# Performance work log

Measured on AMD Instinct MI355X. Metric: run time of the kernel, lower is better.

## Reference

```python
import jax, jax.numpy as jnp
import numpy as np

B, N, FEAT, HID, CTX = 16384, 7, 512, 256, 256
COMB = N * HID + CTX  # 2048


def setup_inputs() -> dict:
    key = jax.random.key(0)
    ks = jax.random.split(key, 20)
    s = lambda k, shape, sc=0.05: jax.random.normal(k, shape, dtype=jnp.float32) * sc
    adj = jax.random.randint(ks[1], (N, N), 0, 2).astype(jnp.float32)
    # guarantee self-loops so no row is fully masked (still exercise nan_to_num path robustly)
    adj = jnp.maximum(adj, jnp.eye(N, dtype=jnp.float32))
    return {
        "node_feats": jax.random.normal(ks[0], (B, N, FEAT), dtype=jnp.float32),
        "adj": adj,
        "context": jax.random.normal(ks[2], (B, CTX), dtype=jnp.float32),
        "base_preds": jax.random.normal(ks[3], (B, 5), dtype=jnp.float32),
        "W1": s(ks[4], (HID, FEAT)),
        "a1": s(ks[5], (1, 2 * HID)),
        "W2": s(ks[6], (HID, HID)),
        "a2": s(ks[7], (1, 2 * HID)),
        "wh1_w": s(ks[8], (32, COMB)), "wh1_b": s(ks[9], (32,)),
        "wh2_w": s(ks[10], (16, 32)), "wh2_b": s(ks[11], (16,)),
        "wh3_w": s(ks[12], (5, 16)), "wh3_b": s(ks[13], (5,)),
        "rh1_w": s(ks[14], (16, COMB)), "rh1_b": s(ks[15], (16,)),
        "rh2_w": s(ks[16], (1, 16)), "rh2_b": s(ks[17], (1,)),
    }


def _gat_layer(x, adj, W, a):
    # x: (B, N, in_dim); W: (D, in_dim); a: (1, 2D)
    h = jnp.einsum('bni,di->bnd', x, W)  # (B, N, D)
    D = W.shape[0]
    # a([h_i, h_j]) == h_i @ a[:, :D] + h_j @ a[:, D:]
    s_i = h @ a[0, :D]   # (B, N)
    s_j = h @ a[0, D:]   # (B, N)
    e = s_i[:, :, None] + s_j[:, None, :]          # (B, N, N)
    e = jax.nn.leaky_relu(e, negative_slope=0.2)
    e = jnp.where(adj[None] == 0, -jnp.inf, e)
    alpha = jax.nn.softmax(e, axis=-1)
    alpha = jnp.nan_to_num(alpha, nan=0.0)
    out = jnp.einsum('bij,bjd->bid', alpha, h)     # (B, N, D)
    return out, alpha


def reference(node_feats, adj, context, base_preds, W1, a1, W2, a2,
              wh1_w, wh1_b, wh2_w, wh2_b, wh3_w, wh3_b,
              rh1_w, rh1_b, rh2_w, rh2_b):
    h, _attn1 = _gat_layer(node_feats, adj, W1, a1)
    h = jax.nn.relu(h)
    h, attn2 = _gat_layer(h, adj, W2, a2)
    h = jax.nn.relu(h)
    graph_embed = h.reshape(h.shape[0], -1)                 # (B, N*D)
    combined = jnp.concatenate([graph_embed, context], -1)  # (B, COMB)
    # weight head (dropout is inference-mode identity)
    t = jax.nn.relu(combined @ wh1_w.T + wh1_b)
    t = jax.nn.relu(t @ wh2_w.T + wh2_b)
    raw_weights = t @ wh3_w.T + wh3_b                       # (B, 5)
    weights = jax.nn.softmax(raw_weights, axis=-1)
    weighted_pred = jnp.sum(weights * base_preds, axis=-1)  # (B,)
    r = jnp.tanh(combined @ rh1_w.T + rh1_b)
    residual = (r @ rh2_w.T + rh2_b)[:, 0] * 0.05
    pred = jnp.maximum(weighted_pred + residual, 0.05)
    return pred, weights, attn2
```

## Files before the change

### kernel.cpp

```cpp
#include <hip/hip_runtime.h>

#define B_SZ 16384
#define NN 7
#define HID 256
#define COMB 2048

typedef __attribute__((ext_vector_type(8))) short short8;
typedef __attribute__((ext_vector_type(4))) float floatx4;
typedef __attribute__((ext_vector_type(4))) unsigned short ushortx4;
typedef unsigned short us;

__device__ __forceinline__ float bf2f(us u) {
    union { unsigned int i; float f; } v; v.i = ((unsigned int)u) << 16; return v.f;
}
__device__ __forceinline__ us f2bf(float f) {
    union { unsigned int i; float f; } v; v.f = f;
    return (us)((v.i + 0x7FFFu + ((v.i >> 16) & 1u)) >> 16);
}
__device__ __forceinline__ us f2bf_fast(float f) {
    union { unsigned int i; float f; } v; v.f = f;
    return (us)((v.i + 0x8000u) >> 16);
}
__device__ __forceinline__ void gl_lds16(const us* g, us* l) {
    __builtin_amdgcn_global_load_lds(
        (const __attribute__((address_space(1))) unsigned int*)g,
        (__attribute__((address_space(3))) unsigned int*)l, 16, 0, 0);
}

__global__ __launch_bounds__(256) void pack_weights(const float* __restrict__ W1,
                                                    const float* __restrict__ W2,
                                                    const float* __restrict__ wh1,
                                                    const float* __restrict__ rh1,
                                                    us* __restrict__ dst) {
    int i = (blockIdx.x * 256 + threadIdx.x) * 4;
    if (i >= 294912) return;
    const float* src; int off;
    if (i < 131072)      { src = W1;  off = i; }
    else if (i < 196608) { src = W2;  off = i - 131072; }
    else if (i < 262144) { src = wh1; off = i - 196608; }
    else                 { src = rh1; off = i - 262144; }
    floatx4 v = *(const floatx4*)(src + off);
    ushortx4 o = {f2bf(v[0]), f2bf(v[1]), f2bf(v[2]), f2bf(v[3])};
    *(ushortx4*)(dst + i) = o;
}

template <int SRC_STRIDE, bool WRITE_ALPHA>
__device__ __forceinline__ void attn_graph(const us* hb, const float* adjs, const float* avec,
                                           us* dst, int dstStride, float* alpha_dst, int lane) {
    float hv[NN][4];
#pragma unroll
    for (int n = 0; n < NN; ++n) {
        ushortx4 r = *(const ushortx4*)(hb + n * SRC_STRIDE + lane * 4);
        hv[n][0] = bf2f(r[0]); hv[n][1] = bf2f(r[1]);
        hv[n][2] = bf2f(r[2]); hv[n][3] = bf2f(r[3]);
    }
    floatx4 ai = *(const floatx4*)(avec + lane * 4);
    floatx4 aj = *(const floatx4*)(avec + HID + lane * 4);
    float si[NN], sj[NN];
#pragma unroll
    for (int n = 0; n < NN; ++n) {
        float pi = hv[n][0] * ai[0] + hv[n][1] * ai[1] + hv[n][2] * ai[2] + hv[n][3] * ai[3];
        float pj = hv[n][0] * aj[0] + hv[n][1] * aj[1] + hv[n][2] * aj[2] + hv[n][3] * aj[3];
#pragma unroll
        for (int off = 32; off; off >>= 1) {
            pi += __shfl_xor(pi, off);
            pj += __shfl_xor(pj, off);
        }
        si[n] = pi; sj[n] = pj;
    }
    const int j = lane & 7;
    float sjm = sj[0];
    if (j == 1) sjm = sj[1];
    if (j == 2) sjm = sj[2];
    if (j == 3) sjm = sj[3];
    if (j == 4) sjm = sj[4];
    if (j == 5) sjm = sj[5];
    if (j == 6) sjm = sj[6];
    const int jc = (j < 7) ? j : 0;
    float alpha[NN];
#pragma unroll
    for (int i = 0; i < NN; ++i) {
        float x = si[i] + sjm;
        x = (x >= 0.f) ? x : 0.2f * x;
        bool ok = (j < 7) && (adjs[i * 7 + jc] != 0.f);
        float e = ok ? x : -1e30f;
        float m = e;
        m = fmaxf(m, __shfl_xor(m, 1, 8));
        m = fmaxf(m, __shfl_xor(m, 2, 8));
        m = fmaxf(m, __shfl_xor(m, 4, 8));
        float ex = ok ? __expf(e - m) : 0.f;
        float s = ex;
        s += __shfl_xor(s, 1, 8);
        s += __shfl_xor(s, 2, 8);
        s += __shfl_xor(s, 4, 8);
        alpha[i] = (s > 0.f) ? ex * __frcp_rn(s) : 0.f;
    }
    if (WRITE_ALPHA && lane < 7) {
#pragma unroll
        for (int i = 0; i < NN; ++i) alpha_dst[i * NN + lane] = alpha[i];
    }
#pragma unroll
    for (int i = 0; i < NN; ++i) {
        floatx4 o = (floatx4){0.f, 0.f, 0.f, 0.f};
#pragma unroll
        for (int jj = 0; jj < NN; ++jj) {
            float a = __shfl(alpha[i], jj, 8);
            o[0] += a * hv[jj][0]; o[1] += a * hv[jj][1];
            o[2] += a * hv[jj][2]; o[3] += a * hv[jj][3];
        }
        ushortx4 st = {f2bf(fmaxf(o[0], 0.f)), f2bf(fmaxf(o[1], 0.f)),
                       f2bf(fmaxf(o[2], 0.f)), f2bf(fmaxf(o[3], 0.f))};
        *(ushortx4*)(dst + i * dstStride + lane * 4) = st;
    }
}


__global__ __launch_bounds__(512, 4) void fused_g1(const float* __restrict__ Af,
                                                   const us* __restrict__ W1b,
                                                   const float* __restrict__ adj,
                                                   const float* __restrict__ avec,
                                                   us* __restrict__ x2g) {
    __shared__ __attribute__((aligned(16))) us As[4096];
    __shared__ __attribute__((aligned(16))) us hs[56 * 264];
    __shared__ float adjs[52];
    const int tid = threadIdx.x;
    const int wave = tid >> 6, lane = tid & 63;
    const int quad = lane >> 4, m16 = lane & 15;
    const long rowBase = (long)blockIdx.x * 56;
    if (tid < 49) adjs[tid] = adj[tid];

    floatx4 acc[4][2];
#pragma unroll
    for (int rt = 0; rt < 4; ++rt)
#pragma unroll
        for (int ct = 0; ct < 2; ++ct) acc[rt][ct] = (floatx4){0.f, 0.f, 0.f, 0.f};

    const int r = tid >> 3, kq8 = tid & 7;
    long rowA = rowBase + r; if (rowA > 114687) rowA = 114687;
    const float* aptr = Af + rowA * 512 + kq8 * 8;
    us* wdst = &As[((r >> 3) * 64 + (r & 7) * 8 + kq8) * 8];
    const int colb = wave * 32;

    for (int s = 0; s < 8; ++s) {
        const int k0 = s * 64;
        floatx4 v0 = *(const floatx4*)(aptr + k0);
        floatx4 v1 = *(const floatx4*)(aptr + k0 + 4);
        short8 sv;
        sv[0] = f2bf_fast(v0[0]); sv[1] = f2bf_fast(v0[1]);
        sv[2] = f2bf_fast(v0[2]); sv[3] = f2bf_fast(v0[3]);
        sv[4] = f2bf_fast(v1[0]); sv[5] = f2bf_fast(v1[1]);
        sv[6] = f2bf_fast(v1[2]); sv[7] = f2bf_fast(v1[3]);
        *(short8*)wdst = sv;
        __syncthreads();
#pragma unroll
        for (int t = 0; t < 2; ++t) {
            short8 b0 = *(const short8*)(W1b + (long)(colb + m16) * 512 + k0 + t * 32 + quad * 8);
            short8 b1 = *(const short8*)(W1b + (long)(colb + 16 + m16) * 512 + k0 + t * 32 + quad * 8);
            short8 a[4];
#pragma unroll
            for (int rt = 0; rt < 4; ++rt)
                a[rt] = *(const short8*)&As[((rt * 2 + (m16 >> 3)) * 64 + (m16 & 7) * 8 + t * 4 + quad) * 8];
#pragma unroll
            for (int rt = 0; rt < 4; ++rt) {
                acc[rt][0] = __builtin_amdgcn_mfma_f32_16x16x32_bf16(a[rt], b0, acc[rt][0], 0, 0, 0);
                acc[rt][1] = __builtin_amdgcn_mfma_f32_16x16x32_bf16(a[rt], b1, acc[rt][1], 0, 0, 0);
            }
        }
        __syncthreads();
    }
#pragma unroll
    for (int rt = 0; rt < 4; ++rt)
#pragma unroll
        for (int ct = 0; ct < 2; ++ct)
#pragma unroll
            for (int i = 0; i < 4; ++i) {
                int row = rt * 16 + quad * 4 + i;
                if (row < 56) hs[row * 264 + wave * 32 + ct * 16 + m16] = f2bf(acc[rt][ct][i]);
            }
    __syncthreads();
    attn_graph<264, false>(&hs[wave * 7 * 264], adjs, avec,
                           x2g + ((long)blockIdx.x * 64 + wave * 7) * 256, 256, nullptr, lane);
}

__global__ __launch_bounds__(512, 4) void fused_rest(const us* __restrict__ x2g,
                                                     const us* __restrict__ W2b,
                                                     const us* __restrict__ Whb,
                                                     const float* __restrict__ adj,
                                                     const float* __restrict__ avec,
                                                     const float* __restrict__ context,
                                                     const float* __restrict__ wh1_b,
                                                     const float* __restrict__ wh2_w,
                                                     const float* __restrict__ wh2_b,
                                                     const float* __restrict__ wh3_w,
                                                     const float* __restrict__ wh3_b,
                                                     const float* __restrict__ rh1_b,
                                                     const float* __restrict__ rh2_w,
                                                     const float* __restrict__ rh2_b,
                                                     const float* __restrict__ base_preds,
                                                     float* __restrict__ out) {
    __shared__ __attribute__((aligned(16))) us As[4096];
    __shared__ __attribute__((aligned(16))) us hs[56 * 264];
    __shared__ __attribute__((aligned(16))) us ctxs[8 * 264];
    __shared__ float red[8 * 384];
    __shared__ float fin[384];
    __shared__ float adjs[52];
    const int tid = threadIdx.x;
    const int wave = tid >> 6, lane = tid & 63;
    const int quad = lane >> 4, m16 = lane & 15;
    const long rowBaseX = (long)blockIdx.x * 64;
    const long gbase = (long)blockIdx.x * 8;
    if (tid < 49) adjs[tid] = adj[tid];
    {
        int cr = tid >> 6, c4 = (tid & 63) * 4;
        floatx4 cv = *(const floatx4*)(context + (gbase + cr) * 256 + c4);
        ushortx4 st = {f2bf(cv[0]), f2bf(cv[1]), f2bf(cv[2]), f2bf(cv[3])};
        *(ushortx4*)&ctxs[cr * 264 + c4] = st;
    }

    floatx4 acc[4][2];
#pragma unroll
    for (int rt = 0; rt < 4; ++rt)
#pragma unroll
        for (int ct = 0; ct < 2; ++ct) acc[rt][ct] = (floatx4){0.f, 0.f, 0.f, 0.f};
    const int colb = wave * 32;

    for (int s = 0; s < 4; ++s) {
        const int k0 = s * 64;
        gl_lds16(x2g + (rowBaseX + wave * 8 + (lane >> 3)) * 256 + k0 + (lane & 7) * 8,
                 &As[wave * 512]);
        __syncthreads();
#pragma unroll
        for (int t = 0; t < 2; ++t) {
            short8 b0 = *(const short8*)(W2b + (long)(colb + m16) * 256 + k0 + t * 32 + quad * 8);
            short8 b1 = *(const short8*)(W2b + (long)(colb + 16 + m16) * 256 + k0 + t * 32 + quad * 8);
            short8 a[4];
#pragma unroll
            for (int rt = 0; rt < 4; ++rt)
                a[rt] = *(const short8*)&As[((rt * 2 + (m16 >> 3)) * 64 + (m16 & 7) * 8 + t * 4 + quad) * 8];
#pragma unroll
            for (int rt = 0; rt < 4; ++rt) {
                acc[rt][0] = __builtin_amdgcn_mfma_f32_16x16x32_bf16(a[rt], b0, acc[rt][0], 0, 0, 0);
                acc[rt][1] = __builtin_amdgcn_mfma_f32_16x16x32_bf16(a[rt], b1, acc[rt][1], 0, 0, 0);
            }
        }
        __syncthreads();
    }
#pragma unroll
    for (int rt = 0; rt < 4; ++rt)
#pragma unroll
        for (int ct = 0; ct < 2; ++ct)
#pragma unroll
            for (int i = 0; i < 4; ++i) {
                int row = rt * 16 + quad * 4 + i;
                if (row < 56) hs[row * 264 + wave * 32 + ct * 16 + m16] = f2bf(acc[rt][ct][i]);
            }
    __syncthreads();
    float* alf = out + 6 * B_SZ;
    attn_graph<264, true>(&hs[wave * 7 * 264], adjs, avec,
                          &hs[wave * 7 * 264], 264, alf + (gbase + wave) * 49, lane);
    __syncthreads();
    floatx4 acc3[3];
#pragma unroll
    for (int ct = 0; ct < 3; ++ct) acc3[ct] = (floatx4){0.f, 0.f, 0.f, 0.f};
    const int g = m16 & 7;
#pragma unroll
    for (int s2 = 0; s2 < 8; ++s2) {
        const int kk = s2 * 32;
        short8 a;
        if (wave < 7) a = *(const short8*)&hs[(g * 7 + wave) * 264 + kk + quad * 8];
        else          a = *(const short8*)&ctxs[g * 264 + kk + quad * 8];
#pragma unroll
        for (int ct = 0; ct < 3; ++ct) {
            short8 bh = *(const short8*)(Whb + (long)(ct * 16 + m16) * COMB + wave * 256 + kk + quad * 8);
            acc3[ct] = __builtin_amdgcn_mfma_f32_16x16x32_bf16(a, bh, acc3[ct], 0, 0, 0);
        }
    }
#pragma unroll
    for (int ct = 0; ct < 3; ++ct)
#pragma unroll
        for (int i = 0; i < 4; ++i) {
            int g2 = quad * 4 + i;
            if (g2 < 8) red[wave * 384 + g2 * 48 + ct * 16 + m16] = acc3[ct][i];
        }
    __syncthreads();
    if (tid < 384) {
        float ssum = 0.f;
#pragma unroll
        for (int w = 0; w < 8; ++w) ssum += red[w * 384 + tid];
        fin[tid] = ssum;
    }
    __syncthreads();
    if (tid < 8) {
        const long b = gbase + tid;
        const float* g48 = &fin[tid * 48];
        float t1[32], r1[16];
#pragma unroll
        for (int k = 0; k < 32; ++k) t1[k] = fmaxf(g48[k] + wh1_b[k], 0.f);
#pragma unroll
        for (int k = 0; k < 16; ++k) r1[k] = tanhf(g48[32 + k] + rh1_b[k]);
        float t2[16];
#pragma unroll
        for (int jj = 0; jj < 16; ++jj) {
            float s = wh2_b[jj];
            for (int k = 0; k < 32; ++k) s += wh2_w[jj * 32 + k] * t1[k];
            t2[jj] = fmaxf(s, 0.f);
        }
        float rw[5], m = -1e30f;
#pragma unroll
        for (int o = 0; o < 5; ++o) {
            float s = wh3_b[o];
            for (int jj = 0; jj < 16; ++jj) s += wh3_w[o * 16 + jj] * t2[jj];
            rw[o] = s; m = fmaxf(m, s);
        }
        float se = 0.f;
#pragma unroll
        for (int o = 0; o < 5; ++o) { rw[o] = __expf(rw[o] - m); se += rw[o]; }
        float inv = 1.f / se, wp = 0.f;
#pragma unroll
        for (int o = 0; o < 5; ++o) {
            float w = rw[o] * inv;
            out[B_SZ + b * 5 + o] = w;
            wp += w * base_preds[b * 5 + o];
        }
        float rs = rh2_b[0];
#pragma unroll
        for (int k = 0; k < 16; ++k) rs += rh2_w[k] * r1[k];
        out[b] = fmaxf(wp + rs * 0.05f, 0.05f);
    }
}

extern "C" void kernel_launch(void* const* d_in, const int* in_sizes, int n_in,
                              void* d_out, int out_size, void* d_ws, size_t ws_size,
                              hipStream_t stream) {
    const float* node_feats = (const float*)d_in[0];
    const float* adj        = (const float*)d_in[1];
    const float* context    = (const float*)d_in[2];
    const float* base_preds = (const float*)d_in[3];
    const float* W1         = (const float*)d_in[4];
    const float* a1         = (const float*)d_in[5];
    const float* W2         = (const float*)d_in[6];
    const float* a2         = (const float*)d_in[7];
    const float* wh1_w = (const float*)d_in[8];
    const float* wh1_b = (const float*)d_in[9];
    const float* wh2_w = (const float*)d_in[10];
    const float* wh2_b = (const float*)d_in[11];
    const float* wh3_w = (const float*)d_in[12];
    const float* wh3_b = (const float*)d_in[13];
    const float* rh1_w = (const float*)d_in[14];
    const float* rh1_b = (const float*)d_in[15];
    const float* rh2_w = (const float*)d_in[16];
    const float* rh2_b = (const float*)d_in[17];
    float* out = (float*)d_out;

    char* ws = (char*)d_ws;
    const size_t X2B = (size_t)2048 * 64 * 256 * 2;
    us* x2  = (us*)ws;
    us* W1b = (us*)(ws + X2B);
    us* W2b = W1b + 131072;
    us* Whb = W2b + 65536;

    pack_weights<<<288, 256, 0, stream>>>(W1, W2, wh1_w, rh1_w, W1b);

    fused_g1<<<2048, 512, 0, stream>>>(node_feats, W1b, adj, a1, x2);

    fused_rest<<<2048, 512, 0, stream>>>(x2, W2b, Whb, adj, a2, context,
                                         wh1_b, wh2_w, wh2_b, wh3_w, wh3_b,
                                         rh1_b, rh2_w, rh2_b, base_preds, out);
}
```

Baseline: 536.7 us.

## Fuse both GAT layers and heads into one kernel with swizzled in-LDS intermediates

Merges the two-kernel pipeline into a single kernel that keeps the layer-1 GAT output in shared memory instead of round-tripping it through a global bf16 buffer. Layer-2 and the head GEMM then read directly from LDS. The shared layout uses XOR swizzling, and the layer-1 A loads are double-buffered and prefetched so one barrier per K step is dropped. Context is converted on the fly, and the tiny MLP tail is parallelised across 64 lanes instead of 8 threads. Risks include higher register and LDS pressure under the new occupancy target, and the long serial chain inside one block.

```diff
diff --git a/kernel.cpp b/kernel.cpp
--- a/kernel.cpp
+++ b/kernel.cpp
@@ -21,10 +21,12 @@
     union { unsigned int i; float f; } v; v.f = f;
     return (us)((v.i + 0x8000u) >> 16);
 }
-__device__ __forceinline__ void gl_lds16(const us* g, us* l) {
-    __builtin_amdgcn_global_load_lds(
-        (const __attribute__((address_space(1))) unsigned int*)g,
-        (__attribute__((address_space(3))) unsigned int*)l, 16, 0, 0);
+
+__device__ __forceinline__ int hoff(int r, int k8) {
+    return ((r >> 3) << 8) | ((r & 7) << 5) | (k8 & 24) | ((k8 ^ r) & 7);
+}
+__device__ __forceinline__ int aoff(int r, int k8) {
+    return ((r >> 3) << 6) | ((r & 7) << 3) | ((k8 ^ r) & 7);
 }
 
 __global__ __launch_bounds__(256) void pack_weights(const float* __restrict__ W1,
@@ -44,15 +46,16 @@
     *(ushortx4*)(dst + i) = o;
 }
 
-template <int SRC_STRIDE, bool WRITE_ALPHA>
-__device__ __forceinline__ void attn_graph(const us* hb, const float* adjs, const float* avec,
-                                           us* dst, int dstStride, float* alpha_dst, int lane) {
+template <bool WRITE_ALPHA>
+__device__ __forceinline__ void attn_graph(us* hs, int r0, const float* adjs, const float* avec,
+                                           float* alpha_dst, int lane) {
+    const int k8 = lane >> 1, sub = (lane & 1) * 4;
     float hv[NN][4];
 #pragma unroll
     for (int n = 0; n < NN; ++n) {
-        ushortx4 r = *(const ushortx4*)(hb + n * SRC_STRIDE + lane * 4);
-        hv[n][0] = bf2f(r[0]); hv[n][1] = bf2f(r[1]);
-        hv[n][2] = bf2f(r[2]); hv[n][3] = bf2f(r[3]);
+        ushortx4 rr = *(const ushortx4*)(hs + hoff(r0 + n, k8) * 8 + sub);
+        hv[n][0] = bf2f(rr[0]); hv[n][1] = bf2f(rr[1]);
+        hv[n][2] = bf2f(rr[2]); hv[n][3] = bf2f(rr[3]);
     }
     floatx4 ai = *(const floatx4*)(avec + lane * 4);
     floatx4 aj = *(const floatx4*)(avec + HID + lane * 4);
@@ -110,24 +113,45 @@
         }
         ushortx4 st = {f2bf(fmaxf(o[0], 0.f)), f2bf(fmaxf(o[1], 0.f)),
                        f2bf(fmaxf(o[2], 0.f)), f2bf(fmaxf(o[3], 0.f))};
-        *(ushortx4*)(dst + i * dstStride + lane * 4) = st;
-    }
-}
-
-
-__global__ __launch_bounds__(512, 4) void fused_g1(const float* __restrict__ Af,
-                                                   const us* __restrict__ W1b,
-                                                   const float* __restrict__ adj,
-                                                   const float* __restrict__ avec,
-                                                   us* __restrict__ x2g) {
-    __shared__ __attribute__((aligned(16))) us As[4096];
-    __shared__ __attribute__((aligned(16))) us hs[56 * 264];
+        *(ushortx4*)(hs + hoff(r0 + i, k8) * 8 + sub) = st;
+    }
+}
+
+__device__ __forceinline__ void cwrite(us* hs, floatx4 (&acc)[4][2], int wave, int quad, int m16) {
+#pragma unroll
+    for (int rt = 0; rt < 4; ++rt)
+#pragma unroll
+        for (int ct = 0; ct < 2; ++ct)
+#pragma unroll
+            for (int i = 0; i < 4; ++i) {
+                int row = rt * 16 + quad * 4 + i;
+                if (row < 56)
+                    hs[hoff(row, wave * 4 + ct * 2 + (m16 >> 3)) * 8 + (m16 & 7)] =
+                        f2bf(acc[rt][ct][i]);
+            }
+}
+
+__global__ __launch_bounds__(512, 6) void fused_all(
+    const float* __restrict__ Af, const us* __restrict__ W1b, const us* __restrict__ W2b,
+    const us* __restrict__ Whb, const float* __restrict__ adj, const float* __restrict__ a1v,
+    const float* __restrict__ a2v, const float* __restrict__ context,
+    const float* __restrict__ wh1_b, const float* __restrict__ wh2_w,
+    const float* __restrict__ wh2_b, const float* __restrict__ wh3_w,
+    const float* __restrict__ wh3_b, const float* __restrict__ rh1_b,
+    const float* __restrict__ rh2_w, const float* __restrict__ rh2_b,
+    const float* __restrict__ base_preds, float* __restrict__ out) {
+    __shared__ __attribute__((aligned(16))) us hs[16384];
+    __shared__ __attribute__((aligned(16))) char ubuf[16384];
     __shared__ float adjs[52];
+    us* As = (us*)ubuf;
+    float* red = (float*)ubuf;
+    float* fin = red + 3072;
     const int tid = threadIdx.x;
     const int wave = tid >> 6, lane = tid & 63;
     const int quad = lane >> 4, m16 = lane & 15;
-    const long rowBase = (long)blockIdx.x * 56;
+    const long gbase = (long)blockIdx.x * 8;
     if (tid < 49) adjs[tid] = adj[tid];
+    *(ushortx4*)(hs + 14336 + tid * 4) = (ushortx4){0, 0, 0, 0};
 
     floatx4 acc[4][2];
 #pragma unroll
@@ -136,22 +160,28 @@
         for (int ct = 0; ct < 2; ++ct) acc[rt][ct] = (floatx4){0.f, 0.f, 0.f, 0.f};
 
     const int r = tid >> 3, kq8 = tid & 7;
-    long rowA = rowBase + r; if (rowA > 114687) rowA = 114687;
+    long rowA = gbase * 7 + r; if (rowA > 114687) rowA = 114687;
     const float* aptr = Af + rowA * 512 + kq8 * 8;
-    us* wdst = &As[((r >> 3) * 64 + (r & 7) * 8 + kq8) * 8];
+    us* wdst = As + aoff(r, kq8) * 8;
     const int colb = wave * 32;
 
+    floatx4 v0 = *(const floatx4*)aptr;
+    floatx4 v1 = *(const floatx4*)(aptr + 4);
+#pragma unroll
     for (int s = 0; s < 8; ++s) {
-        const int k0 = s * 64;
-        floatx4 v0 = *(const floatx4*)(aptr + k0);
-        floatx4 v1 = *(const floatx4*)(aptr + k0 + 4);
         short8 sv;
         sv[0] = f2bf_fast(v0[0]); sv[1] = f2bf_fast(v0[1]);
         sv[2] = f2bf_fast(v0[2]); sv[3] = f2bf_fast(v0[3]);
         sv[4] = f2bf_fast(v1[0]); sv[5] = f2bf_fast(v1[1]);
         sv[6] = f2bf_fast(v1[2]); sv[7] = f2bf_fast(v1[3]);
-        *(short8*)wdst = sv;
+        if (s < 7) {
+            v0 = *(const floatx4*)(aptr + (s + 1) * 64);
+            v1 = *(const floatx4*)(aptr + (s + 1) * 64 + 4);
+        }
+        *(short8*)(wdst + (s & 1) * 4096) = sv;
         __syncthreads();
+        const us* Ab = As + (s & 1) * 4096;
+        const int k0 = s * 64;
 #pragma unroll
         for (int t = 0; t < 2; ++t) {
             short8 b0 = *(const short8*)(W1b + (long)(colb + m16) * 512 + k0 + t * 32 + quad * 8);
@@ -159,76 +189,26 @@
             short8 a[4];
 #pragma unroll
             for (int rt = 0; rt < 4; ++rt)
-                a[rt] = *(const short8*)&As[((rt * 2 + (m16 >> 3)) * 64 + (m16 & 7) * 8 + t * 4 + quad) * 8];
+                a[rt] = *(const short8*)(Ab + aoff(rt * 16 + m16, t * 4 + quad) * 8);
 #pragma unroll
             for (int rt = 0; rt < 4; ++rt) {
                 acc[rt][0] = __builtin_amdgcn_mfma_f32_16x16x32_bf16(a[rt], b0, acc[rt][0], 0, 0, 0);
                 acc[rt][1] = __builtin_amdgcn_mfma_f32_16x16x32_bf16(a[rt], b1, acc[rt][1], 0, 0, 0);
             }
         }
-        __syncthreads();
-    }
+    }
+    cwrite(hs, acc, wave, quad, m16);
+    __syncthreads();
+    attn_graph<false>(hs, wave * NN, adjs, a1v, nullptr, lane);
+    __syncthreads();
+
 #pragma unroll
     for (int rt = 0; rt < 4; ++rt)
 #pragma unroll
-        for (int ct = 0; ct < 2; ++ct)
-#pragma unroll
-            for (int i = 0; i < 4; ++i) {
-                int row = rt * 16 + quad * 4 + i;
-                if (row < 56) hs[row * 264 + wave * 32 + ct * 16 + m16] = f2bf(acc[rt][ct][i]);
-            }
-    __syncthreads();
-    attn_graph<264, false>(&hs[wave * 7 * 264], adjs, avec,
-                           x2g + ((long)blockIdx.x * 64 + wave * 7) * 256, 256, nullptr, lane);
-}
-
-__global__ __launch_bounds__(512, 4) void fused_rest(const us* __restrict__ x2g,
-                                                     const us* __restrict__ W2b,
-                                                     const us* __restrict__ Whb,
-                                                     const float* __restrict__ adj,
-                                                     const float* __restrict__ avec,
-                                                     const float* __restrict__ context,
-                                                     const float* __restrict__ wh1_b,
-                                                     const float* __restrict__ wh2_w,
-                                                     const float* __restrict__ wh2_b,
-                                                     const float* __restrict__ wh3_w,
-                                                     const float* __restrict__ wh3_b,
-                                                     const float* __restrict__ rh1_b,
-                                                     const float* __restrict__ rh2_w,
-                                                     const float* __restrict__ rh2_b,
-                                                     const float* __restrict__ base_preds,
-                                                     float* __restrict__ out) {
-    __shared__ __attribute__((aligned(16))) us As[4096];
-    __shared__ __attribute__((aligned(16))) us hs[56 * 264];
-    __shared__ __attribute__((aligned(16))) us ctxs[8 * 264];
-    __shared__ float red[8 * 384];
-    __shared__ float fin[384];
-    __shared__ float adjs[52];
-    const int tid = threadIdx.x;
-    const int wave = tid >> 6, lane = tid & 63;
-    const int quad = lane >> 4, m16 = lane & 15;
-    const long rowBaseX = (long)blockIdx.x * 64;
-    const long gbase = (long)blockIdx.x * 8;
-    if (tid < 49) adjs[tid] = adj[tid];
-    {
-        int cr = tid >> 6, c4 = (tid & 63) * 4;
-        floatx4 cv = *(const floatx4*)(context + (gbase + cr) * 256 + c4);
-        ushortx4 st = {f2bf(cv[0]), f2bf(cv[1]), f2bf(cv[2]), f2bf(cv[3])};
-        *(ushortx4*)&ctxs[cr * 264 + c4] = st;
-    }
-
-    floatx4 acc[4][2];
-#pragma unroll
-    for (int rt = 0; rt < 4; ++rt)
-#pragma unroll
         for (int ct = 0; ct < 2; ++ct) acc[rt][ct] = (floatx4){0.f, 0.f, 0.f, 0.f};
-    const int colb = wave * 32;
-
+#pragma unroll
     for (int s = 0; s < 4; ++s) {
         const int k0 = s * 64;
-        gl_lds16(x2g + (rowBaseX + wave * 8 + (lane >> 3)) * 256 + k0 + (lane & 7) * 8,
-                 &As[wave * 512]);
-        __syncthreads();
 #pragma unroll
         for (int t = 0; t < 2; ++t) {
             short8 b0 = *(const short8*)(W2b + (long)(colb + m16) * 256 + k0 + t * 32 + quad * 8);
@@ -236,29 +216,20 @@
             short8 a[4];
 #pragma unroll
             for (int rt = 0; rt < 4; ++rt)
-                a[rt] = *(const short8*)&As[((rt * 2 + (m16 >> 3)) * 64 + (m16 & 7) * 8 + t * 4 + quad) * 8];
+                a[rt] = *(const short8*)(hs + hoff(rt * 16 + m16, s * 8 + t * 4 + quad) * 8);
 #pragma unroll
             for (int rt = 0; rt < 4; ++rt) {
                 acc[rt][0] = __builtin_amdgcn_mfma_f32_16x16x32_bf16(a[rt], b0, acc[rt][0], 0, 0, 0);
                 acc[rt][1] = __builtin_amdgcn_mfma_f32_16x16x32_bf16(a[rt], b1, acc[rt][1], 0, 0, 0);
             }
         }
-        __syncthreads();
-    }
-#pragma unroll
-    for (int rt = 0; rt < 4; ++rt)
-#pragma unroll
-        for (int ct = 0; ct < 2; ++ct)
-#pragma unroll
-            for (int i = 0; i < 4; ++i) {
-                int row = rt * 16 + quad * 4 + i;
-                if (row < 56) hs[row * 264 + wave * 32 + ct * 16 + m16] = f2bf(acc[rt][ct][i]);
-            }
-    __syncthreads();
-    float* alf = out + 6 * B_SZ;
-    attn_graph<264, true>(&hs[wave * 7 * 264], adjs, avec,
-                          &hs[wave * 7 * 264], 264, alf + (gbase + wave) * 49, lane);
-    __syncthreads();
+    }
+    __syncthreads();
+    cwrite(hs, acc, wave, quad, m16);
+    __syncthreads();
+    attn_graph<true>(hs, wave * NN, adjs, a2v, out + 6 * B_SZ + (gbase + wave) * 49, lane);
+    __syncthreads();
+
     floatx4 acc3[3];
 #pragma unroll
     for (int ct = 0; ct < 3; ++ct) acc3[ct] = (floatx4){0.f, 0.f, 0.f, 0.f};
@@ -267,8 +238,17 @@
     for (int s2 = 0; s2 < 8; ++s2) {
         const int kk = s2 * 32;
         short8 a;
-        if (wave < 7) a = *(const short8*)&hs[(g * 7 + wave) * 264 + kk + quad * 8];
-        else          a = *(const short8*)&ctxs[g * 264 + kk + quad * 8];
+        if (wave < 7) {
+            a = *(const short8*)(hs + hoff(g * NN + wave, s2 * 4 + quad) * 8);
+        } else {
+            const float* cp = context + (gbase + g) * 256 + kk + quad * 8;
+            floatx4 c0 = *(const floatx4*)cp;
+            floatx4 c1 = *(const floatx4*)(cp + 4);
+            a[0] = (short)f2bf(c0[0]); a[1] = (short)f2bf(c0[1]);
+            a[2] = (short)f2bf(c0[2]); a[3] = (short)f2bf(c0[3]);
+            a[4] = (short)f2bf(c1[0]); a[5] = (short)f2bf(c1[1]);
+            a[6] = (short)f2bf(c1[2]); a[7] = (short)f2bf(c1[3]);
+        }
 #pragma unroll
         for (int ct = 0; ct < 3; ++ct) {
             short8 bh = *(const short8*)(Whb + (long)(ct * 16 + m16) * COMB + wave * 256 + kk + quad * 8);
@@ -290,42 +270,71 @@
         fin[tid] = ssum;
     }
     __syncthreads();
-    if (tid < 8) {
-        const long b = gbase + tid;
-        const float* g48 = &fin[tid * 48];
-        float t1[32], r1[16];
-#pragma unroll
-        for (int k = 0; k < 32; ++k) t1[k] = fmaxf(g48[k] + wh1_b[k], 0.f);
-#pragma unroll
-        for (int k = 0; k < 16; ++k) r1[k] = tanhf(g48[32 + k] + rh1_b[k]);
-        float t2[16];
-#pragma unroll
-        for (int jj = 0; jj < 16; ++jj) {
-            float s = wh2_b[jj];
-            for (int k = 0; k < 32; ++k) s += wh2_w[jj * 32 + k] * t1[k];
-            t2[jj] = fmaxf(s, 0.f);
-        }
-        float rw[5], m = -1e30f;
-#pragma unroll
-        for (int o = 0; o < 5; ++o) {
-            float s = wh3_b[o];
-            for (int jj = 0; jj < 16; ++jj) s += wh3_w[o * 16 + jj] * t2[jj];
-            rw[o] = s; m = fmaxf(m, s);
-        }
-        float se = 0.f;
-#pragma unroll
-        for (int o = 0; o < 5; ++o) { rw[o] = __expf(rw[o] - m); se += rw[o]; }
-        float inv = 1.f / se, wp = 0.f;
-#pragma unroll
-        for (int o = 0; o < 5; ++o) {
-            float w = rw[o] * inv;
-            out[B_SZ + b * 5 + o] = w;
-            wp += w * base_preds[b * 5 + o];
-        }
-        float rs = rh2_b[0];
-#pragma unroll
-        for (int k = 0; k < 16; ++k) rs += rh2_w[k] * r1[k];
-        out[b] = fmaxf(wp + rs * 0.05f, 0.05f);
+
+    const int fj = lane & 7, fg = lane >> 3;
+    const long fb = gbase + fg;
+    float rp = 0.f;
+    float* t1s = red;
+    float* t2s = red + 256;
+    if (tid < 64) {
+        const float* g48 = fin + fg * 48;
+#pragma unroll
+        for (int x = 0; x < 4; ++x) {
+            int k = fj * 4 + x;
+            t1s[fg * 32 + k] = fmaxf(g48[k] + wh1_b[k], 0.f);
+        }
+#pragma unroll
+        for (int x = 0; x < 2; ++x) {
+            int k = fj * 2 + x;
+            float rv = tanhf(g48[32 + k] + rh1_b[k]);
+            rp += rh2_w[k] * rv;
+        }
+    }
+    __syncthreads();
+    if (tid < 64) {
+        float s0 = wh2_b[fj * 2], s1 = wh2_b[fj * 2 + 1];
+#pragma unroll
+        for (int k = 0; k < 32; ++k) {
+            float tv = t1s[fg * 32 + k];
+            s0 += wh2_w[(fj * 2) * 32 + k] * tv;
+            s1 += wh2_w[(fj * 2 + 1) * 32 + k] * tv;
+        }
+        t2s[fg * 16 + fj * 2] = fmaxf(s0, 0.f);
+        t2s[fg * 16 + fj * 2 + 1] = fmaxf(s1, 0.f);
+    }
+    __syncthreads();
+    if (tid < 64) {
+        float rw = -1e30f;
+        if (fj < 5) {
+            float s = wh3_b[fj];
+#pragma unroll
+            for (int k = 0; k < 16; ++k) s += wh3_w[fj * 16 + k] * t2s[fg * 16 + k];
+            rw = s;
+        }
+        float m = rw;
+        m = fmaxf(m, __shfl_xor(m, 1, 8));
+        m = fmaxf(m, __shfl_xor(m, 2, 8));
+        m = fmaxf(m, __shfl_xor(m, 4, 8));
+        float e = (fj < 5) ? __expf(rw - m) : 0.f;
+        float se = e;
+        se += __shfl_xor(se, 1, 8);
+        se += __shfl_xor(se, 2, 8);
+        se += __shfl_xor(se, 4, 8);
+        float inv = 1.f / se;
+        float wp = 0.f;
+        if (fj < 5) {
+            float w = e * inv;
+            out[B_SZ + fb * 5 + fj] = w;
+            wp = w * base_preds[fb * 5 + fj];
+        }
+        wp += __shfl_xor(wp, 1, 8);
+        wp += __shfl_xor(wp, 2, 8);
+        wp += __shfl_xor(wp, 4, 8);
+        float rs = rp;
+        rs += __shfl_xor(rs, 1, 8);
+        rs += __shfl_xor(rs, 2, 8);
+        rs += __shfl_xor(rs, 4, 8);
+        if (fj == 0) out[fb] = fmaxf(wp + (rs + rh2_b[0]) * 0.05f, 0.05f);
     }
 }
 
@@ -353,17 +362,13 @@
     float* out = (float*)d_out;
 
     char* ws = (char*)d_ws;
-    const size_t X2B = (size_t)2048 * 64 * 256 * 2;
-    us* x2  = (us*)ws;
-    us* W1b = (us*)(ws + X2B);
+    us* W1b = (us*)ws;
     us* W2b = W1b + 131072;
     us* Whb = W2b + 65536;
 
     pack_weights<<<288, 256, 0, stream>>>(W1, W2, wh1_w, rh1_w, W1b);
 
-    fused_g1<<<2048, 512, 0, stream>>>(node_feats, W1b, adj, a1, x2);
-
-    fused_rest<<<2048, 512, 0, stream>>>(x2, W2b, Whb, adj, a2, context,
-                                         wh1_b, wh2_w, wh2_b, wh3_w, wh3_b,
-                                         rh1_b, rh2_w, rh2_b, base_preds, out);
-}
+    fused_all<<<2048, 512, 0, stream>>>(node_feats, W1b, W2b, Whb, adj, a1, a2, context,
+                                        wh1_b, wh2_w, wh2_b, wh3_w, wh3_b,
+                                        rh1_b, rh2_w, rh2_b, base_preds, out);
+}
```

Measured after the change: 572.8 us. 1.07x slower.
